# Performance work log

Hardware: AMD Instinct MI355X
Metric: run time of the kernel (lower is better)

Reference implementation:

```python
import jax, jax.numpy as jnp
import numpy as np

LS, BS, N_HID, N_ENS = 1, 32, 256, 64
SEQ, D_IN, M_OBS = 64, 256, 64


def setup_inputs() -> dict:
    key = jax.random.key(0)
    ks = jax.random.split(key, 10)
    s = 1.0 / np.sqrt(N_HID)
    return {
        "x": jax.random.normal(ks[0], (BS, SEQ, D_IN), jnp.float32),
        "y": jax.random.normal(ks[1], (BS, M_OBS), jnp.float32),
        "enkf_state": jax.random.normal(ks[2], (LS, BS, N_HID, N_ENS), jnp.float32),
        "W_ih": jax.random.normal(ks[3], (D_IN, 4 * N_HID), jnp.float32) * s,
        "W_hh": jax.random.normal(ks[4], (N_HID, 4 * N_HID), jnp.float32) * s,
        "b": jnp.zeros((4 * N_HID,), jnp.float32),
        "Wh": jax.random.normal(ks[5], (M_OBS, N_HID), jnp.float32) * s,
        "bh": jnp.zeros((M_OBS,), jnp.float32),
        "q": jnp.asarray(1.0, jnp.float32),
        "e": jnp.asarray(0.1, jnp.float32),
        "r": jnp.asarray(0.5, jnp.float32),
        "eps_h": jax.random.normal(ks[6], (N_ENS // 2, LS, BS, N_HID), jnp.float32),
        "eps_c": jax.random.normal(ks[7], (N_ENS // 2, LS, BS, N_HID), jnp.float32),
        "train": 1,
    }


def reference(x, y, enkf_state, W_ih, W_hh, b, Wh, bh, q, e, r, eps_h, eps_c, train):
    ls, bs, n, N = enkf_state.shape
    mid = N // 2
    nq = jnp.sqrt(q * q)  # noise std = sqrt(q^2), keeps q differentiable in graph
    ne = jnp.sqrt(e * e)

    # ---- forecast: LSTM transition per ensemble member (vmapped, ls == 1) ----
    xs = jnp.swapaxes(x, 0, 1)  # [seq, bs, d_in]

    def lstm_member(h0, c0, eh, ec):  # h0,c0: [ls,bs,n]
        def step(carry, xt):
            h, c = carry
            g = xt @ W_ih + h @ W_hh + b  # [bs, 4n]
            i, f, gg, o = jnp.split(g, 4, axis=-1)
            c2 = jax.nn.sigmoid(f) * c + jax.nn.sigmoid(i) * jnp.tanh(gg)
            h2 = jax.nn.sigmoid(o) * jnp.tanh(c2)
            return (h2, c2), None
        (hT, cT), _ = jax.lax.scan(step, (h0[0], c0[0]), xs)
        return (hT + nq * eh[0])[None], (cT + ne * ec[0])[None]

    h0s = jnp.moveaxis(enkf_state[..., :mid], -1, 0)  # [mid, ls, bs, n]
    c0s = jnp.moveaxis(enkf_state[..., mid:], -1, 0)
    hN, cN = jax.vmap(lstm_member)(h0s, c0s, eps_h, eps_c)
    state = jnp.moveaxis(jnp.concatenate([hN, cN], axis=0), 0, -1)  # [ls,bs,n,N]

    eye_m = jnp.eye(M_OBS, dtype=state.dtype)

    def obs(s):  # observation model on last LSTM layer: [bs, m, N]
        return jnp.einsum('mn,bnN->bmN', Wh, s[-1]) + bh[:, None]

    def estimate(hxi):
        mu = hxi.mean(-1)  # [bs, m]
        cd = hxi - mu[..., None]
        cov = cd @ jnp.swapaxes(cd, -1, -2) / (N - 1) + eye_m * (r * r)
        return mu, cov

    def enkf_update(s):
        hxi = obs(s)
        hx, P = estimate(hxi)
        HA = hxi - hx[..., None]               # [bs, m, N]
        A = s - s.mean(-1)[..., None]          # [ls, bs, n, N]
        innov = y[:, :, None] - hxi            # [bs, m, N]
        sol = jnp.linalg.solve(P, innov)       # inv(P) @ innov
        G = jnp.einsum('lbnN,bmN->lbnm', A, HA)
        return s + jnp.einsum('lbnm,bmN->lbnN', G, sol) / (N - 1)

    def loglik_nis(mu, sig):
        S = sig + 1e-6 * eye_m
        L = jnp.linalg.cholesky(S)
        innov = y - mu
        v = jax.scipy.linalg.cho_solve((L, True), innov[..., None])[..., 0]
        quad = jnp.sum(innov * v, axis=-1)  # innov^T S^{-1} innov per batch
        logdet = 2.0 * jnp.sum(jnp.log(jnp.diagonal(L, axis1=-2, axis2=-1)), axis=-1)
        l = jnp.sum(-0.5 * logdet - 0.5 * quad)
        nis = jnp.mean(quad)
        return l, nis

    if train:  # training branch: filter first, then estimate on filtered ensemble
        state = enkf_update(state)
        mu, sig = estimate(obs(state))
        l, nis = loglik_nis(mu, sig)
        return mu, sig, state, l, nis
    else:      # eval branch: estimate on forecast, then filter
        mu, sig = estimate(obs(state))
        l, nis = loglik_nis(mu, sig)
        state = enkf_update(state)
        return mu, sig, state, l, nis
```

## Files before the change

kernel.cpp:

```cpp
#include <hip/hip_runtime.h>
#include <hip/hip_bf16.h>


typedef _Float16 f16;
typedef _Float16 f16x8 __attribute__((ext_vector_type(8)));
typedef _Float16 h4 __attribute__((ext_vector_type(4)));
typedef float f32x4 __attribute__((ext_vector_type(4)));

#define BS   32
#define NH   256
#define NE   64
#define SEQQ 64
#define DIN  256
#define MOBS 64
#define G4   1024

__device__ __forceinline__ float fast_sigmoid(float x) {
  return __builtin_amdgcn_rcpf(1.f + __expf(-x));
}
__device__ __forceinline__ float fast_tanh(float x) {
  return 2.f * __builtin_amdgcn_rcpf(1.f + __expf(-2.f * x)) - 1.f;
}

__global__ __launch_bounds__(256)
void k_pack(const float* __restrict__ W_hh, const float* __restrict__ W_ih,
            const float* __restrict__ Wh, f16* __restrict__ Wpack,
            f16* __restrict__ WpackIh, f16* __restrict__ WhfP) {
  const int blk = blockIdx.x, tid = threadIdx.x;
  if (blk < 32) {
    const float* src = (blk & 1) ? W_ih : W_hh;
    f16* dst = (blk & 1) ? WpackIh : Wpack;
    const int kh = blk >> 1;
    __shared__ f16 ls[16][1032];
    for (int idx = tid; idx < 16 * 1024; idx += 256) {
      int kr = idx >> 10, n2 = idx & 1023;
      ls[kr][n2] = (f16)src[(size_t)(kh * 16 + kr) * G4 + n2];
    }
    __syncthreads();
    const int ks = kh >> 1;
    const int lane = tid & 63;
    const int qd = lane >> 4, c0 = lane & 15;
    if ((qd >> 1) == (kh & 1)) {
      const int krow = (qd & 1) * 8;
      for (int tile = tid >> 6; tile < 64; tile += 4) {
        f16x8 v;
#pragma unroll
        for (int j = 0; j < 8; ++j) v[j] = ls[krow + j][tile * 16 + c0];
        *(f16x8*)&dst[(size_t)((tile * 8 + ks) * 64 + lane) * 8] = v;
      }
    }
  } else {
    for (int g = tid; g < 2048; g += 256) {
      int lane = g & 63, ks = (g >> 6) & 7, mt = g >> 9;
      int row = mt * 16 + (lane & 15);
      int k0 = ks * 32 + (lane >> 4) * 8;
#pragma unroll
      for (int j = 0; j < 8; ++j)
        WhfP[g * 8 + j] = (f16)Wh[row * NH + k0 + j];
    }
  }
}

__global__ __launch_bounds__(512, 2)
void k_xw(const float* __restrict__ x, const f16* __restrict__ WpackIh,
          const float* __restrict__ bv, h4* __restrict__ xwH) {
  __shared__ __align__(16) f16 xs[16 * 264];
  const int tid = threadIdx.x;
  const int m0 = blockIdx.x * 16;
  const int b = m0 >> 6, t0 = m0 & 63;
  const int g4 = b >> 4, br = b & 15;
  const int lane = tid & 63, w = tid >> 6;
  const int c0 = lane & 15, qd = lane >> 4;
  const int w0 = w * 32;
  for (int idx = tid; idx < 16 * 256; idx += 512) {
    int r = idx >> 8, k = idx & 255;
    xs[r * 264 + k] = (f16)x[(size_t)(m0 + r) * 256 + k];
  }
  __syncthreads();
  f16x8 afr[8];
#pragma unroll
  for (int ks = 0; ks < 8; ++ks)
    afr[ks] = *(const f16x8*)&xs[c0 * 264 + ks * 32 + qd * 8];
  const f16* wp0 = WpackIh + (size_t)lane * 8;
  f32x4 acc[8];
#pragma unroll
  for (int tt = 0; tt < 8; ++tt) {
    const int tg = ((tt >> 1) << 4) + w * 2 + (tt & 1);
    const f16* p = wp0 + (size_t)tg * 4096;
    f16x8 bf[8];
#pragma unroll
    for (int ks = 0; ks < 8; ++ks) bf[ks] = *(const f16x8*)(p + ks * 512);
    f32x4 a0 = {0.f, 0.f, 0.f, 0.f}, a1 = {0.f, 0.f, 0.f, 0.f};
#pragma unroll
    for (int ks = 0; ks < 8; ks += 2) {
      a0 = __builtin_amdgcn_mfma_f32_16x16x32_f16(afr[ks], bf[ks], a0, 0, 0, 0);
      a1 = __builtin_amdgcn_mfma_f32_16x16x32_f16(afr[ks + 1], bf[ks + 1], a1, 0, 0, 0);
    }
    acc[tt] = a0 + a1;
  }
#pragma unroll
  for (int nt = 0; nt < 2; ++nt) {
    const int j = w0 + nt * 16 + c0;
#pragma unroll
    for (int q = 0; q < 4; ++q) {
      const int t = t0 + qd * 4 + q;
      h4 v;
      v[0] = (f16)(acc[0 + nt][q] + bv[j]);
      v[1] = (f16)(acc[2 + nt][q] + bv[256 + j]);
      v[2] = (f16)(acc[4 + nt][q] + bv[512 + j]);
      v[3] = (f16)(acc[6 + nt][q] + bv[768 + j]);
      xwH[((size_t)(g4 * 64 + t) * 16 + br) * 256 + j] = v;
    }
  }
}

template <bool LAST>
__device__ __forceinline__ void lstm_step(
    int t, const f16* hcur, f16* hnxt, const f16* wg0, const f16* wg1,
    const f16* gbase, const f16x8 (&wres)[8], int c0, int qd, int j, int b0,
    int e, const h4* xwbase, f16x8 (&bf)[2][2], float (&creg)[4],
    const float* __restrict__ eps_h, const float* __restrict__ eps_c,
    float nq, float nee, float* __restrict__ stateF2) {
  h4 xw[4];
#pragma unroll
  for (int q = 0; q < 4; ++q)
    xw[q] = xwbase[(size_t)(t * 16 + qd * 4 + q) * 256 + j];

  f32x4 acc0 = {0.f, 0.f, 0.f, 0.f}, acc1 = {0.f, 0.f, 0.f, 0.f};
  f32x4 acc2 = {0.f, 0.f, 0.f, 0.f}, acc3 = {0.f, 0.f, 0.f, 0.f};
#pragma unroll
  for (int ks = 0; ks < 8; ++ks) {
    f16x8 afr = *(const f16x8*)&hcur[c0 * 264 + ks * 32 + qd * 8];
    f16x8 gbf = *(const f16x8*)(gbase + ks * 512);
    const int k2 = (ks + 1) & 7;
    bf[(ks + 1) & 1][0] = *(const f16x8*)(wg0 + k2 * 512);
    bf[(ks + 1) & 1][1] = *(const f16x8*)(wg1 + k2 * 512);
    acc0 = __builtin_amdgcn_mfma_f32_16x16x32_f16(afr, bf[ks & 1][0], acc0, 0, 0, 0);
    acc1 = __builtin_amdgcn_mfma_f32_16x16x32_f16(afr, bf[ks & 1][1], acc1, 0, 0, 0);
    acc2 = __builtin_amdgcn_mfma_f32_16x16x32_f16(afr, gbf, acc2, 0, 0, 0);
    acc3 = __builtin_amdgcn_mfma_f32_16x16x32_f16(afr, wres[ks], acc3, 0, 0, 0);
  }

#pragma unroll
  for (int q = 0; q < 4; ++q) {
    const int r = qd * 4 + q;
    float iv = acc0[q] + (float)xw[q][0];
    float fv = acc1[q] + (float)xw[q][1];
    float gv = acc2[q] + (float)xw[q][2];
    float ov = acc3[q] + (float)xw[q][3];
    float c2 = fast_sigmoid(fv) * creg[q] + fast_sigmoid(iv) * fast_tanh(gv);
    float h2 = fast_sigmoid(ov) * fast_tanh(c2);
    creg[q] = c2;
    if (!LAST) {
      hnxt[r * 264 + j] = (f16)h2;
    } else {
      stateF2[((size_t)e * 32 + b0 + r) * 256 + j] =
          h2 + nq * eps_h[(e * BS + b0 + r) * NH + j];
      stateF2[((size_t)(32 + e) * 32 + b0 + r) * 256 + j] =
          c2 + nee * eps_c[(e * BS + b0 + r) * NH + j];
    }
  }
  if (!LAST) __syncthreads();
}

__global__ __launch_bounds__(1024)
void k_lstm(const h4* __restrict__ xwH, const f16* __restrict__ Wpack,
            const float* __restrict__ enkf, const float* __restrict__ eps_h,
            const float* __restrict__ eps_c, const float* __restrict__ qp,
            const float* __restrict__ ep, float* __restrict__ stateF2) {
  __shared__ __align__(16) f16 glds[65536];
  __shared__ __align__(16) f16 hs[2][16 * 264];
  const int tid = threadIdx.x;
  const int e = blockIdx.x >> 1;
  const int g4 = blockIdx.x & 1;
  const int b0 = g4 * 16;
  const int lane = tid & 63;
  const int ws = tid >> 6;
  const int c0 = lane & 15;
  const int qd = lane >> 4;
  const int j = ws * 16 + c0;

  {
    const f16* gsrc = Wpack + 32 * 4096;
    for (int i = tid; i < 8192; i += 1024)
      *(f16x8*)&glds[i * 8] = *(const f16x8*)&gsrc[(size_t)i * 8];
  }
  f16x8 wres[8];
  {
    const f16* op = Wpack + (size_t)(48 + ws) * 4096 + (size_t)lane * 8;
#pragma unroll
    for (int ks = 0; ks < 8; ++ks) wres[ks] = *(const f16x8*)(op + ks * 512);
  }
  for (int idx = tid; idx < 16 * 256; idx += 1024) {
    int r = idx >> 8, nh = idx & 255;
    hs[0][r * 264 + nh] = (f16)enkf[((b0 + r) * NH + nh) * NE + e];
  }
  float creg[4];
#pragma unroll
  for (int q = 0; q < 4; ++q)
    creg[q] = enkf[((b0 + qd * 4 + q) * NH + j) * NE + 32 + e];

  const float nq = fabsf(qp[0]);
  const float nee = fabsf(ep[0]);

  const f16* wg0 = Wpack + (size_t)(0 * 16 + ws) * 4096 + (size_t)lane * 8;
  const f16* wg1 = Wpack + (size_t)(1 * 16 + ws) * 4096 + (size_t)lane * 8;
  const f16* gbase = glds + (size_t)ws * 4096 + (size_t)lane * 8;

  f16x8 bf[2][2];
  bf[0][0] = *(const f16x8*)(wg0);
  bf[0][1] = *(const f16x8*)(wg1);

  const h4* xwbase = xwH + (size_t)g4 * 64 * 16 * 256;
  __syncthreads();

  for (int t = 0; t < 62; t += 2) {
    lstm_step<false>(t, hs[0], hs[1], wg0, wg1, gbase, wres, c0, qd, j, b0, e,
                     xwbase, bf, creg, eps_h, eps_c, nq, nee, stateF2);
    lstm_step<false>(t + 1, hs[1], hs[0], wg0, wg1, gbase, wres, c0, qd, j, b0,
                     e, xwbase, bf, creg, eps_h, eps_c, nq, nee, stateF2);
  }
  lstm_step<false>(62, hs[0], hs[1], wg0, wg1, gbase, wres, c0, qd, j, b0, e,
                   xwbase, bf, creg, eps_h, eps_c, nq, nee, stateF2);
  lstm_step<true>(63, hs[1], hs[0], wg0, wg1, gbase, wres, c0, qd, j, b0, e,
                  xwbase, bf, creg, eps_h, eps_c, nq, nee, stateF2);
}

__global__ __launch_bounds__(256)
void k_fused(const float* __restrict__ stateF2, const f16* __restrict__ WhfP,
             const float* __restrict__ bh, const float* __restrict__ rp,
             const float* __restrict__ y, float* __restrict__ mu_out,
             float* __restrict__ sig_out, float* __restrict__ state_out,
             float* __restrict__ quad_g, float* __restrict__ logdet_g) {
  __shared__ __align__(16) f16 stT[64 * 264];
  __shared__ float hxl[64 * 66];
  __shared__ float Pm[64 * 65];
  __shared__ __align__(16) f16 TT[64 * 72];
  __shared__ __align__(16) char U[36864];
  __shared__ float hxm[64];
  __shared__ float dinv[64];
  __shared__ float srm[256];

  const int tid = threadIdx.x, b = blockIdx.x;
  const int lane = tid & 63, wave = tid >> 6;
  const int c0 = lane & 15, qd = lane >> 4;
  const int n = tid & 63, mg = tid >> 6;
  const float r2 = rp[0] * rp[0];

  f16x8 whfr[8];
#pragma unroll
  for (int ks = 0; ks < 8; ++ks)
    whfr[ks] = *(const f16x8*)&WhfP[(((size_t)wave * 8 + ks) * 64 + lane) * 8];

  for (int idx = tid; idx < NH * NE; idx += 256) {
    int j = idx >> 8, k = idx & 255;
    stT[j * 264 + k] = (f16)stateF2[((size_t)j * 32 + b) * 256 + k];
  }
  __syncthreads();
  for (int nt = 0; nt < 4; ++nt) {
    f32x4 acc = {0.f, 0.f, 0.f, 0.f};
#pragma unroll
    for (int ks = 0; ks < 8; ++ks) {
      f16x8 bfr = *(const f16x8*)&stT[(nt * 16 + c0) * 264 + ks * 32 + qd * 8];
      acc = __builtin_amdgcn_mfma_f32_16x16x32_f16(whfr[ks], bfr, acc, 0, 0, 0);
    }
#pragma unroll
    for (int q = 0; q < 4; ++q)
      hxl[(wave * 16 + qd * 4 + q) * 66 + nt * 16 + c0] = acc[q] + bh[wave * 16 + qd * 4 + q];
  }
  __syncthreads();
  if (tid < 64) {
    float s = 0.f;
    for (int j = 0; j < 64; ++j) s += hxl[tid * 66 + j];
    hxm[tid] = s * (1.f / 64.f);
  }
  __syncthreads();
  {
    f16* HAf = (f16*)U;
    for (int idx = tid; idx < 4096; idx += 256) {
      int m = idx >> 6, j = idx & 63;
      HAf[m * 72 + j] = (f16)(hxl[m * 66 + j] - hxm[m]);
    }
    __syncthreads();
    f16x8 afr[2];
#pragma unroll
    for (int ks = 0; ks < 2; ++ks)
      afr[ks] = *(const f16x8*)&HAf[(wave * 16 + c0) * 72 + ks * 32 + qd * 8];
    for (int nt = 0; nt < 4; ++nt) {
      f32x4 acc = {0.f, 0.f, 0.f, 0.f};
#pragma unroll
      for (int ks = 0; ks < 2; ++ks) {
        f16x8 bfr = *(const f16x8*)&HAf[(nt * 16 + c0) * 72 + ks * 32 + qd * 8];
        acc = __builtin_amdgcn_mfma_f32_16x16x32_f16(afr[ks], bfr, acc, 0, 0, 0);
      }
#pragma unroll
      for (int q = 0; q < 4; ++q) {
        int m1 = wave * 16 + qd * 4 + q, m2 = nt * 16 + c0;
        Pm[m1 * 65 + m2] = acc[q] * (1.f / 63.f) + (m1 == m2 ? r2 : 0.f);
      }
    }
  }
  __syncthreads();

  {
    float* R = (float*)U;
    f16* HAT = (f16*)(U + 16384);
    f16* solT = (f16*)(U + 25600);
    for (int idx = tid; idx < 4096; idx += 256) {
      int m = idx >> 6, j = idx & 63;
      float hv = hxl[m * 66 + j];
      R[idx] = y[b * 64 + m] - hv;
      HAT[j * 72 + m] = (f16)(hv - hxm[m]);
    }
    __syncthreads();
    for (int k = 0; k < 64; ++k) {
      float dk = Pm[k * 65 + k];
      if (n > k) {
        float f = Pm[n * 65 + k] * __builtin_amdgcn_rcpf(dk);
        for (int m = k + 1 + mg; m < 64; m += 4)
          Pm[m * 65 + n] -= Pm[m * 65 + k] * f;
      }
      __syncthreads();
    }
    if (tid < 64) dinv[tid] = __builtin_amdgcn_rcpf(Pm[tid * 65 + tid]);
    __syncthreads();
    for (int i0 = 0; i0 < 64; i0 += 8) {
      if (wave == 0) {
        float rl[8];
#pragma unroll
        for (int d = 0; d < 8; ++d) rl[d] = R[(i0 + d) * 64 + n];
#pragma unroll
        for (int a = 1; a < 8; ++a)
#pragma unroll
          for (int bq = 0; bq < a; ++bq)
            rl[a] -= Pm[(i0 + a) * 65 + i0 + bq] * dinv[i0 + bq] * rl[bq];
#pragma unroll
        for (int d = 1; d < 8; ++d) R[(i0 + d) * 64 + n] = rl[d];
      }
      __syncthreads();
      for (int m = i0 + 8 + mg; m < 64; m += 4) {
        float s = R[m * 64 + n];
#pragma unroll
        for (int d = 0; d < 8; ++d)
          s -= Pm[m * 65 + i0 + d] * dinv[i0 + d] * R[(i0 + d) * 64 + n];
        R[m * 64 + n] = s;
      }
      __syncthreads();
    }
    for (int idx = tid; idx < 4096; idx += 256) R[idx] *= dinv[idx >> 6];
    __syncthreads();
    for (int i0 = 56; i0 >= 0; i0 -= 8) {
      if (wave == 0) {
        float rl[8];
#pragma unroll
        for (int d = 0; d < 8; ++d) rl[d] = R[(i0 + d) * 64 + n];
#pragma unroll
        for (int a = 6; a >= 0; --a)
#pragma unroll
          for (int bq = 7; bq > a; --bq)
            rl[a] -= Pm[(i0 + bq) * 65 + i0 + a] * dinv[i0 + a] * rl[bq];
#pragma unroll
        for (int d = 0; d < 7; ++d) R[(i0 + d) * 64 + n] = rl[d];
      }
      __syncthreads();
      for (int m = mg; m < i0; m += 4) {
        float s = R[m * 64 + n];
        float dm = dinv[m];
#pragma unroll
        for (int d = 0; d < 8; ++d)
          s -= Pm[(i0 + d) * 65 + m] * dm * R[(i0 + d) * 64 + n];
        R[m * 64 + n] = s;
      }
      __syncthreads();
    }
    for (int idx = tid; idx < 4096; idx += 256) {
      int m = idx >> 6, j = idx & 63;
      solT[j * 72 + m] = (f16)R[m * 64 + j];
    }
    __syncthreads();
    f16x8 afr[2];
#pragma unroll
    for (int ks = 0; ks < 2; ++ks)
      afr[ks] = *(const f16x8*)&HAT[(wave * 16 + c0) * 72 + ks * 32 + qd * 8];
    for (int nt = 0; nt < 4; ++nt) {
      f32x4 acc = {0.f, 0.f, 0.f, 0.f};
#pragma unroll
      for (int ks = 0; ks < 2; ++ks) {
        f16x8 bfr = *(const f16x8*)&solT[(nt * 16 + c0) * 72 + ks * 32 + qd * 8];
        acc = __builtin_amdgcn_mfma_f32_16x16x32_f16(afr[ks], bfr, acc, 0, 0, 0);
      }
#pragma unroll
      for (int q = 0; q < 4; ++q) {
        int jp = wave * 16 + qd * 4 + q, j = nt * 16 + c0;
        TT[j * 72 + jp] = (f16)(acc[q] * (1.f / 63.f));
      }
    }
  }
  __syncthreads();

  {
    f16* Af = (f16*)U;
    for (int idx = tid; idx < NH * NE; idx += 256) {
      int j = idx >> 8, k = idx & 255;
      Af[k * 72 + j] = (f16)stateF2[((size_t)j * 32 + b) * 256 + k];
    }
    __syncthreads();
    {
      float s = 0.f;
      for (int j = 0; j < 64; ++j) s += (float)Af[tid * 72 + j];
      srm[tid] = s * (1.f / 64.f);
    }
    __syncthreads();
    for (int idx = tid; idx < NH * NE; idx += 256) {
      int nh = idx >> 6, j = idx & 63;
      Af[nh * 72 + j] = (f16)((float)Af[nh * 72 + j] - srm[nh]);
    }
    __syncthreads();
    f16x8 bfr[4][2];
#pragma unroll
    for (int nt = 0; nt < 4; ++nt)
#pragma unroll
      for (int ks = 0; ks < 2; ++ks)
        bfr[nt][ks] = *(const f16x8*)&TT[(nt * 16 + c0) * 72 + ks * 32 + qd * 8];
    for (int mt0 = 0; mt0 < 4; ++mt0) {
      int mt = wave * 4 + mt0;
      f16x8 afr[2];
#pragma unroll
      for (int ks = 0; ks < 2; ++ks)
        afr[ks] = *(const f16x8*)&Af[(mt * 16 + c0) * 72 + ks * 32 + qd * 8];
#pragma unroll
      for (int nt = 0; nt < 4; ++nt) {
        f32x4 acc = {0.f, 0.f, 0.f, 0.f};
#pragma unroll
        for (int ks = 0; ks < 2; ++ks)
          acc = __builtin_amdgcn_mfma_f32_16x16x32_f16(afr[ks], bfr[nt][ks], acc, 0, 0, 0);
#pragma unroll
        for (int q = 0; q < 4; ++q) {
          int m = mt * 16 + qd * 4 + q, j = nt * 16 + c0;
          float v = (float)Af[m * 72 + j] + srm[m] + acc[q];
          state_out[b * (NH * NE) + m * 64 + j] = v;
          stT[j * 264 + m] = (f16)v;
        }
      }
    }
  }
  __syncthreads();

  for (int nt = 0; nt < 4; ++nt) {
    f32x4 acc = {0.f, 0.f, 0.f, 0.f};
#pragma unroll
    for (int ks = 0; ks < 8; ++ks) {
      f16x8 bfr = *(const f16x8*)&stT[(nt * 16 + c0) * 264 + ks * 32 + qd * 8];
      acc = __builtin_amdgcn_mfma_f32_16x16x32_f16(whfr[ks], bfr, acc, 0, 0, 0);
    }
#pragma unroll
    for (int q = 0; q < 4; ++q)
      hxl[(wave * 16 + qd * 4 + q) * 66 + nt * 16 + c0] = acc[q] + bh[wave * 16 + qd * 4 + q];
  }
  __syncthreads();
  if (tid < 64) {
    float s = 0.f;
    for (int j = 0; j < 64; ++j) s += hxl[tid * 66 + j];
    s *= (1.f / 64.f);
    hxm[tid] = s;
    mu_out[b * MOBS + tid] = s;
  }
  __syncthreads();
  {
    f16* HAf = (f16*)U;
    for (int idx = tid; idx < 4096; idx += 256) {
      int m = idx >> 6, j = idx & 63;
      HAf[m * 72 + j] = (f16)(hxl[m * 66 + j] - hxm[m]);
    }
    __syncthreads();
    f16x8 afr[2];
#pragma unroll
    for (int ks = 0; ks < 2; ++ks)
      afr[ks] = *(const f16x8*)&HAf[(wave * 16 + c0) * 72 + ks * 32 + qd * 8];
    for (int nt = 0; nt < 4; ++nt) {
      f32x4 acc = {0.f, 0.f, 0.f, 0.f};
#pragma unroll
      for (int ks = 0; ks < 2; ++ks) {
        f16x8 bfr = *(const f16x8*)&HAf[(nt * 16 + c0) * 72 + ks * 32 + qd * 8];
        acc = __builtin_amdgcn_mfma_f32_16x16x32_f16(afr[ks], bfr, acc, 0, 0, 0);
      }
#pragma unroll
      for (int q = 0; q < 4; ++q) {
        int m1 = wave * 16 + qd * 4 + q, m2 = nt * 16 + c0;
        float v = acc[q] * (1.f / 63.f) + (m1 == m2 ? r2 : 0.f);
        sig_out[b * (MOBS * MOBS) + m1 * MOBS + m2] = v;
        Pm[m1 * 65 + m2] = v + (m1 == m2 ? 1e-6f : 0.f);
      }
    }
  }
  __syncthreads();

  for (int k = 0; k < 64; ++k) {
    float dk = Pm[k * 65 + k];
    if (n > k) {
      float f = Pm[n * 65 + k] * __builtin_amdgcn_rcpf(dk);
      for (int m = k + 1 + mg; m < 64; m += 4)
        Pm[m * 65 + n] -= Pm[m * 65 + k] * f;
    }
    __syncthreads();
  }
  if (tid < 64) dinv[tid] = __builtin_amdgcn_rcpf(Pm[tid * 65 + tid]);
  __syncthreads();
  if (wave == 0) {
    const int m = lane;
    float rm = y[b * 64 + m] - hxm[m];
    const float r0 = rm;
    for (int i = 0; i < 63; ++i) {
      float xi = __shfl(rm, i);
      if (m > i) rm -= Pm[m * 65 + i] * dinv[i] * xi;
    }
    rm *= dinv[m];
    for (int i = 63; i >= 1; --i) {
      float xi = __shfl(rm, i);
      if (m < i) rm -= Pm[i * 65 + m] * dinv[m] * xi;
    }
    float prod = r0 * rm;
    float ld = __logf(Pm[m * 65 + m]);
#pragma unroll
    for (int off = 32; off; off >>= 1) {
      prod += __shfl_down(prod, off);
      ld += __shfl_down(ld, off);
    }
    if (m == 0) {
      quad_g[b] = prod;
      logdet_g[b] = ld;
    }
  }
}

__global__ __launch_bounds__(64)
void k_reduce(const float* __restrict__ quad_g, const float* __restrict__ logdet_g,
              float* __restrict__ out_l, float* __restrict__ out_nis) {
  if (threadIdx.x == 0 && blockIdx.x == 0) {
    float l = 0.f, qs = 0.f;
    for (int b2 = 0; b2 < 32; ++b2) {
      l += -0.5f * (logdet_g[b2] + quad_g[b2]);
      qs += quad_g[b2];
    }
    out_l[0] = l;
    out_nis[0] = qs * (1.f / 32.f);
  }
}

extern "C" void kernel_launch(void* const* d_in, const int* in_sizes, int n_in,
                              void* d_out, int out_size, void* d_ws, size_t ws_size,
                              hipStream_t stream) {
  (void)in_sizes; (void)n_in; (void)out_size; (void)ws_size;
  const float* x     = (const float*)d_in[0];
  const float* y     = (const float*)d_in[1];
  const float* enkf  = (const float*)d_in[2];
  const float* W_ih  = (const float*)d_in[3];
  const float* W_hh  = (const float*)d_in[4];
  const float* bvec  = (const float*)d_in[5];
  const float* Wh    = (const float*)d_in[6];
  const float* bh    = (const float*)d_in[7];
  const float* qp    = (const float*)d_in[8];
  const float* ep    = (const float*)d_in[9];
  const float* rp    = (const float*)d_in[10];
  const float* eps_h = (const float*)d_in[11];
  const float* eps_c = (const float*)d_in[12];

  char* ws = (char*)d_ws;
  h4*    xwH     = (h4*)(ws);
  f16*   Wpack   = (f16*)(ws + 4194304);
  f16*   WpackIh = (f16*)(ws + 4718592);
  f16*   WhfP    = (f16*)(ws + 5242880);
  float* stateF2 = (float*)(ws + 5275648);
  float* quadg   = (float*)(ws + 7372800);
  float* ldg     = (float*)(ws + 7372928);

  float* out = (float*)d_out;
  float* mu_out    = out;
  float* sig_out   = out + 2048;
  float* state_out = out + 133120;
  float* l_out     = out + 657408;
  float* nis_out   = out + 657409;

  k_pack<<<33, 256, 0, stream>>>(W_hh, W_ih, Wh, Wpack, WpackIh, WhfP);
  k_xw<<<128, 512, 0, stream>>>(x, WpackIh, bvec, xwH);
  k_lstm<<<64, 1024, 0, stream>>>(xwH, Wpack, enkf, eps_h, eps_c, qp, ep, stateF2);
  k_fused<<<32, 256, 0, stream>>>(stateF2, WhfP, bh, rp, y, mu_out, sig_out,
                                  state_out, quadg, ldg);
  k_reduce<<<1, 64, 0, stream>>>(quadg, ldg, l_out, nis_out);
}
```

Before: 457.4 us.

## Block the LDL factorization by 8 columns and fold the final reduction into atomics

```diff
diff --git a/kernel.cpp b/kernel.cpp
--- a/kernel.cpp
+++ b/kernel.cpp
@@ -22,10 +22,53 @@
   return 2.f * __builtin_amdgcn_rcpf(1.f + __expf(-2.f * x)) - 1.f;
 }
 
+__device__ __forceinline__ void ldl_factor8(float* Pm, int tid) {
+  const int lane = tid & 63, wave = tid >> 6;
+  for (int kb = 0; kb < 64; kb += 8) {
+    if (wave == 0) {
+      float rl[8];
+#pragma unroll
+      for (int d = 0; d < 8; ++d) rl[d] = Pm[lane * 65 + kb + d];
+#pragma unroll
+      for (int kk = 0; kk < 8; ++kk) {
+        float dk = __shfl(rl[kk], kb + kk);
+        float fm = rl[kk] * __builtin_amdgcn_rcpf(dk);
+#pragma unroll
+        for (int jj = kk + 1; jj < 8; ++jj) {
+          float cj = __shfl(rl[kk], kb + jj);
+          if (lane > kb + kk) rl[jj] -= fm * cj;
+        }
+      }
+#pragma unroll
+      for (int d = 0; d < 8; ++d)
+        if (lane >= kb) Pm[lane * 65 + kb + d] = rl[d];
+    }
+    __syncthreads();
+    if (kb < 56) {
+      const int n = lane;
+      if (n >= kb + 8) {
+        float ln[8];
+#pragma unroll
+        for (int d = 0; d < 8; ++d)
+          ln[d] = Pm[n * 65 + kb + d] *
+                  __builtin_amdgcn_rcpf(Pm[(kb + d) * 65 + kb + d]);
+        for (int m = kb + 8 + wave; m < 64; m += 4) {
+          float s = Pm[m * 65 + n];
+#pragma unroll
+          for (int d = 0; d < 8; ++d) s -= Pm[m * 65 + kb + d] * ln[d];
+          Pm[m * 65 + n] = s;
+        }
+      }
+      __syncthreads();
+    }
+  }
+}
+
 __global__ __launch_bounds__(256)
 void k_pack(const float* __restrict__ W_hh, const float* __restrict__ W_ih,
             const float* __restrict__ Wh, f16* __restrict__ Wpack,
-            f16* __restrict__ WpackIh, f16* __restrict__ WhfP) {
+            f16* __restrict__ WpackIh, f16* __restrict__ WhfP,
+            float* __restrict__ l_out, float* __restrict__ nis_out) {
   const int blk = blockIdx.x, tid = threadIdx.x;
   if (blk < 32) {
     const float* src = (blk & 1) ? W_ih : W_hh;
@@ -50,6 +93,7 @@
       }
     }
   } else {
+    if (tid == 0) { l_out[0] = 0.f; nis_out[0] = 0.f; }
     for (int g = tid; g < 2048; g += 256) {
       int lane = g & 63, ks = (g >> 6) & 7, mt = g >> 9;
       int row = mt * 16 + (lane & 15);
@@ -231,7 +275,7 @@
              const float* __restrict__ bh, const float* __restrict__ rp,
              const float* __restrict__ y, float* __restrict__ mu_out,
              float* __restrict__ sig_out, float* __restrict__ state_out,
-             float* __restrict__ quad_g, float* __restrict__ logdet_g) {
+             float* __restrict__ l_out, float* __restrict__ nis_out) {
   __shared__ __align__(16) f16 stT[64 * 264];
   __shared__ float hxl[64 * 66];
   __shared__ float Pm[64 * 65];
@@ -313,15 +357,7 @@
       HAT[j * 72 + m] = (f16)(hv - hxm[m]);
     }
     __syncthreads();
-    for (int k = 0; k < 64; ++k) {
-      float dk = Pm[k * 65 + k];
-      if (n > k) {
-        float f = Pm[n * 65 + k] * __builtin_amdgcn_rcpf(dk);
-        for (int m = k + 1 + mg; m < 64; m += 4)
-          Pm[m * 65 + n] -= Pm[m * 65 + k] * f;
-      }
-      __syncthreads();
-    }
+    ldl_factor8(Pm, tid);
     if (tid < 64) dinv[tid] = __builtin_amdgcn_rcpf(Pm[tid * 65 + tid]);
     __syncthreads();
     for (int i0 = 0; i0 < 64; i0 += 8) {
@@ -495,15 +531,7 @@
   }
   __syncthreads();
 
-  for (int k = 0; k < 64; ++k) {
-    float dk = Pm[k * 65 + k];
-    if (n > k) {
-      float f = Pm[n * 65 + k] * __builtin_amdgcn_rcpf(dk);
-      for (int m = k + 1 + mg; m < 64; m += 4)
-        Pm[m * 65 + n] -= Pm[m * 65 + k] * f;
-    }
-    __syncthreads();
-  }
+  ldl_factor8(Pm, tid);
   if (tid < 64) dinv[tid] = __builtin_amdgcn_rcpf(Pm[tid * 65 + tid]);
   __syncthreads();
   if (wave == 0) {
@@ -527,23 +555,9 @@
       ld += __shfl_down(ld, off);
     }
     if (m == 0) {
-      quad_g[b] = prod;
-      logdet_g[b] = ld;
-    }
-  }
-}
-
-__global__ __launch_bounds__(64)
-void k_reduce(const float* __restrict__ quad_g, const float* __restrict__ logdet_g,
-              float* __restrict__ out_l, float* __restrict__ out_nis) {
-  if (threadIdx.x == 0 && blockIdx.x == 0) {
-    float l = 0.f, qs = 0.f;
-    for (int b2 = 0; b2 < 32; ++b2) {
-      l += -0.5f * (logdet_g[b2] + quad_g[b2]);
-      qs += quad_g[b2];
-    }
-    out_l[0] = l;
-    out_nis[0] = qs * (1.f / 32.f);
+      atomicAdd(l_out, -0.5f * (ld + prod));
+      atomicAdd(nis_out, prod * (1.f / 32.f));
+    }
   }
 }
 
@@ -571,8 +585,6 @@
   f16*   WpackIh = (f16*)(ws + 4718592);
   f16*   WhfP    = (f16*)(ws + 5242880);
   float* stateF2 = (float*)(ws + 5275648);
-  float* quadg   = (float*)(ws + 7372800);
-  float* ldg     = (float*)(ws + 7372928);
 
   float* out = (float*)d_out;
   float* mu_out    = out;
@@ -581,10 +593,10 @@
   float* l_out     = out + 657408;
   float* nis_out   = out + 657409;
 
-  k_pack<<<33, 256, 0, stream>>>(W_hh, W_ih, Wh, Wpack, WpackIh, WhfP);
+  k_pack<<<33, 256, 0, stream>>>(W_hh, W_ih, Wh, Wpack, WpackIh, WhfP,
+                                 l_out, nis_out);
   k_xw<<<128, 512, 0, stream>>>(x, WpackIh, bvec, xwH);
   k_lstm<<<64, 1024, 0, stream>>>(xwH, Wpack, enkf, eps_h, eps_c, qp, ep, stateF2);
   k_fused<<<32, 256, 0, stream>>>(stateF2, WhfP, bh, rp, y, mu_out, sig_out,
-                                  state_out, quadg, ldg);
-  k_reduce<<<1, 64, 0, stream>>>(quadg, ldg, l_out, nis_out);
-}
+                                  state_out, l_out, nis_out);
+}
```

Result: faster. 416.1 us (-9.0%).
